# Kernel optimization log

Measured on AMD Instinct MI355X. Metric: run time of the kernel, lower is better.

Reference implementation:

```python
import jax, jax.numpy as jnp
import numpy as np

N_NODES = 64
KS = (52, 42, 34)  # ceil(0.8*64), ceil(0.8*52), ceil(0.8*42)


def _gcn(x, A, W, b):
    # GCNConv(improved=True): self-loop fill 2.0, symmetric normalization. A[tgt, src], weighted.
    n = A.shape[0]
    Ah = A + 2.0 * jnp.eye(n, dtype=A.dtype)
    d = Ah.sum(-1)
    dis = jnp.where(d > 0, jax.lax.rsqrt(d), 0.0)
    An = dis[:, None] * Ah * dis[None, :]
    return An @ (x @ W) + b


def _augment(A):
    # GraphUNet.augment_adj: add self loops (weight 1), A2 = A1 @ A1, remove self loops
    n = A.shape[0]
    eye = jnp.eye(n, dtype=A.dtype)
    A1 = A + eye
    return (A1 @ A1) * (1.0 - eye)


def _pool(x, A, w, k):
    # TopKPooling: score = tanh(x.w/||w||), keep top-k, scale kept features by score
    s = jnp.tanh((x @ w) / jnp.linalg.norm(w))
    sv, perm = jax.lax.top_k(s, k)
    return x[perm] * sv[:, None], A[perm][:, perm], perm


def _unet(x, A, dw0, db0, dws, dbs, pws, uws, ubs, uwl, ubl):
    # GraphUNet(depth=3, sum_res=True), single graph: x [n, F2], A [n, n]
    x = jax.nn.relu(_gcn(x, A, dw0, db0))
    xs, As, perms = [x], [A], []
    for i in range(3):
        A = _augment(A)
        x, A, perm = _pool(x, A, pws[i], KS[i])
        x = jax.nn.relu(_gcn(x, A, dws[i], dbs[i]))
        if i < 2:
            xs.append(x)
            As.append(A)
        perms.append(perm)
    for i in range(3):
        j = 2 - i
        res, Aj, perm = xs[j], As[j], perms[j]
        x = res + jnp.zeros_like(res).at[perm].set(x)
        if i < 2:
            x = jax.nn.relu(_gcn(x, Aj, uws[i], ubs[i]))
        else:
            x = _gcn(x, Aj, uwl, ubl)
    return x


def _nnconv(x, src, dst, ea, mw, mb, rw, bias):
    # NNConv(aggr='mean'): per-edge MLP weight, gather-matmul-scatter-mean + root + bias
    B, E = src.shape
    fin, fout = rw.shape
    We = jax.nn.relu(ea @ mw + mb).reshape(B, E, fin, fout)  # [B,E,fin,fout]
    xs = jnp.take_along_axis(x, src[..., None], axis=1)      # [B,E,fin]
    msg = jnp.einsum('bei,beio->beo', xs, We)                # [B,E,fout]
    seg = jax.vmap(lambda m, d: jax.ops.segment_sum(m, d, num_segments=N_NODES))
    sums = seg(msg, dst)
    cnt = seg(jnp.ones(msg.shape[:2] + (1,), msg.dtype), dst)
    agg = sums / jnp.maximum(cnt, 1.0)
    return agg + x @ rw + bias


def _adj(src, dst):
    A = jnp.zeros((N_NODES, N_NODES), jnp.float32).at[dst, src].set(1.0)
    return A * (1.0 - jnp.eye(N_NODES, dtype=jnp.float32))


def _branch(x, ei, ea, mlp1, mlp2, u1, u2):
    src, dst = ei[:, 0], ei[:, 1]
    A = jax.vmap(_adj)(src, dst)
    x = jax.nn.relu(_nnconv(x, src, dst, ea, *mlp1))
    x = jax.nn.relu(jax.vmap(lambda h, a: _unet(h, a, *u1))(x, A))
    x = jax.nn.relu(_nnconv(x, src, dst, ea, *mlp2))
    x = jax.nn.relu(jax.vmap(lambda h, a: _unet(h, a, *u2))(x, A))
    return x.mean(axis=1)  # global_mean_pool (equal-sized graphs)


def setup_inputs() -> dict:
    key = jax.random.key(0)
    keys = iter(jax.random.split(key, 64))
    def nrm(shape, s=1.0):
        return jax.random.normal(next(keys), shape, jnp.float32) * s
    B, n, E, F, F2, Q, H, C = 128, 64, 512, 64, 32, 16, 256, 50
    inp = {}
    inp['x1'] = nrm((B, n, F))
    inp['ei1'] = jax.random.randint(next(keys), (B, 2, E), 0, n, jnp.int32)
    inp['ea1'] = jax.random.uniform(next(keys), (B, E, 1), jnp.float32)
    inp['jw1'] = nrm((B, Q))
    inp['x2'] = nrm((B, n, F))
    inp['ei2'] = jax.random.randint(next(keys), (B, 2, E), 0, n, jnp.int32)
    inp['ea2'] = jax.random.uniform(next(keys), (B, E, 1), jnp.float32)
    inp['jw2'] = nrm((B, Q))
    inp['m1w'] = nrm((1, F * F2), 0.1)
    inp['m1b'] = nrm((F * F2,), 0.1)
    inp['r1w'] = nrm((F, F2), 0.1)
    inp['c1b'] = nrm((F2,), 0.1)
    inp['m2w'] = nrm((1, F2 * F2), 0.1)
    inp['m2b'] = nrm((F2 * F2,), 0.1)
    inp['r2w'] = nrm((F2, F2), 0.1)
    inp['c2b'] = nrm((F2,), 0.1)
    for p in ('u1', 'u2'):
        inp[p + '_dw0'] = nrm((F2, C), 0.1)
        inp[p + '_db0'] = nrm((C,), 0.1)
        inp[p + '_dws'] = nrm((3, C, C), 0.1)
        inp[p + '_dbs'] = nrm((3, C), 0.1)
        inp[p + '_pws'] = nrm((3, C), 0.1)
        inp[p + '_uws'] = nrm((2, C, C), 0.1)
        inp[p + '_ubs'] = nrm((2, C), 0.1)
        inp[p + '_uwl'] = nrm((C, F2), 0.1)
        inp[p + '_ubl'] = nrm((F2,), 0.1)
    inp['bb_w'] = nrm(((F2 + Q) * 2, H), 0.1)
    inp['bb_b'] = nrm((H,), 0.1)
    return inp


def reference(x1, ei1, ea1, jw1, x2, ei2, ea2, jw2,
              m1w, m1b, r1w, c1b, m2w, m2b, r2w, c2b,
              u1_dw0, u1_db0, u1_dws, u1_dbs, u1_pws, u1_uws, u1_ubs, u1_uwl, u1_ubl,
              u2_dw0, u2_db0, u2_dws, u2_dbs, u2_pws, u2_uws, u2_ubs, u2_uwl, u2_ubl,
              bb_w, bb_b):
    mlp1 = (m1w, m1b, r1w, c1b)
    mlp2 = (m2w, m2b, r2w, c2b)
    u1 = (u1_dw0, u1_db0, u1_dws, u1_dbs, u1_pws, u1_uws, u1_ubs, u1_uwl, u1_ubl)
    u2 = (u2_dw0, u2_db0, u2_dws, u2_dbs, u2_pws, u2_uws, u2_ubs, u2_uwl, u2_ubl)
    r1 = _branch(x1, ei1, ea1, mlp1, mlp2, u1, u2)
    r2 = _branch(x2, ei2, ea2, mlp1, mlp2, u1, u2)
    c = jnp.concatenate([r1, jw1, r2, jw2], axis=1)  # [(F2+Q)*2]
    return jax.nn.relu(c @ bb_w + bb_b)
```

## Files before the change

kernel.cpp:

```cpp
#include <hip/hip_runtime.h>
#include <math.h>

#define UT 1024
#define XS 52
#define ASTR 66

__device__ __forceinline__ float wred16(float v) {
    v += __shfl_xor(v, 8); v += __shfl_xor(v, 4);
    v += __shfl_xor(v, 2); v += __shfl_xor(v, 1);
    return v;
}

__device__ __forceinline__ void gcn_u(int n, int cin, int cout,
    float* __restrict__ x, float* __restrict__ tmp,
    const float* __restrict__ A, float* __restrict__ Wl,
    float* __restrict__ dis,
    const float* __restrict__ Wg, const float* __restrict__ bg, bool relu)
{
    const int tid = threadIdx.x;
    const int nso = (cout + 3) >> 2;
    for (int idx = tid; idx < 51 * 52; idx += UT) {
        int r = idx / 52, c = idx - r * 52;
        float v = 0.f;
        if (r < cin && c < cout) v = Wg[r * cout + c];
        else if (r == 50 && c < cout) v = bg[c];
        Wl[idx] = v;
    }
    {
        int r = tid >> 4, l = tid & 15;
        float s = 0.f;
        if (r < n) for (int j = l; j < n; j += 16) s += A[r * ASTR + j];
        s = wred16(s);
        if (l == 0 && r < n) dis[r] = 1.0f / sqrtf(2.0f + s);
    }
    __syncthreads();
    const int nr2 = n >> 1;
    const int items = nr2 * nso;
    for (int it = tid; it < items; it += UT) {
        int i0 = (it / nso) * 2, o0 = (it - (it / nso) * nso) * 4;
        float a0=0,a1=0,a2=0,a3=0, b0=0,b1=0,b2=0,b3=0;
        float c0=0,c1=0,c2=0,c3=0, d0=0,d1=0,d2=0,d3=0;
        for (int k = 0; k < cin; k += 2) {
            float4 w0 = *(const float4*)&Wl[k * 52 + o0];
            float4 w1 = *(const float4*)&Wl[(k + 1) * 52 + o0];
            float2 xa = *(const float2*)&x[i0 * XS + k];
            float2 xb = *(const float2*)&x[(i0 + 1) * XS + k];
            a0 = fmaf(xa.x, w0.x, a0); a1 = fmaf(xa.x, w0.y, a1);
            a2 = fmaf(xa.x, w0.z, a2); a3 = fmaf(xa.x, w0.w, a3);
            b0 = fmaf(xa.y, w1.x, b0); b1 = fmaf(xa.y, w1.y, b1);
            b2 = fmaf(xa.y, w1.z, b2); b3 = fmaf(xa.y, w1.w, b3);
            c0 = fmaf(xb.x, w0.x, c0); c1 = fmaf(xb.x, w0.y, c1);
            c2 = fmaf(xb.x, w0.z, c2); c3 = fmaf(xb.x, w0.w, c3);
            d0 = fmaf(xb.y, w1.x, d0); d1 = fmaf(xb.y, w1.y, d1);
            d2 = fmaf(xb.y, w1.z, d2); d3 = fmaf(xb.y, w1.w, d3);
        }
        float e0 = dis[i0], e1 = dis[i0 + 1];
        float4 t0, t1;
        t0.x = (a0 + b0) * e0; t0.y = (a1 + b1) * e0;
        t0.z = (a2 + b2) * e0; t0.w = (a3 + b3) * e0;
        t1.x = (c0 + d0) * e1; t1.y = (c1 + d1) * e1;
        t1.z = (c2 + d2) * e1; t1.w = (c3 + d3) * e1;
        *(float4*)&tmp[i0 * XS + o0] = t0;
        *(float4*)&tmp[(i0 + 1) * XS + o0] = t1;
    }
    __syncthreads();
    for (int it = tid; it < items; it += UT) {
        int i0 = (it / nso) * 2, o0 = (it - (it / nso) * nso) * 4;
        float a0=0,a1=0,a2=0,a3=0, b0=0,b1=0,b2=0,b3=0;
        float c0=0,c1=0,c2=0,c3=0, d0=0,d1=0,d2=0,d3=0;
        for (int j = 0; j < n; j += 2) {
            float4 t0 = *(const float4*)&tmp[j * XS + o0];
            float4 t1 = *(const float4*)&tmp[(j + 1) * XS + o0];
            float2 Aa2 = *(const float2*)&A[i0 * ASTR + j];
            float2 Ab2 = *(const float2*)&A[(i0 + 1) * ASTR + j];
            a0 = fmaf(Aa2.x, t0.x, a0); a1 = fmaf(Aa2.x, t0.y, a1);
            a2 = fmaf(Aa2.x, t0.z, a2); a3 = fmaf(Aa2.x, t0.w, a3);
            b0 = fmaf(Aa2.y, t1.x, b0); b1 = fmaf(Aa2.y, t1.y, b1);
            b2 = fmaf(Aa2.y, t1.z, b2); b3 = fmaf(Aa2.y, t1.w, b3);
            c0 = fmaf(Ab2.x, t0.x, c0); c1 = fmaf(Ab2.x, t0.y, c1);
            c2 = fmaf(Ab2.x, t0.z, c2); c3 = fmaf(Ab2.x, t0.w, c3);
            d0 = fmaf(Ab2.y, t1.x, d0); d1 = fmaf(Ab2.y, t1.y, d1);
            d2 = fmaf(Ab2.y, t1.z, d2); d3 = fmaf(Ab2.y, t1.w, d3);
        }
        float4 bias = *(const float4*)&Wl[50 * 52 + o0];
        float4 s0 = *(const float4*)&tmp[i0 * XS + o0];
        float4 s1 = *(const float4*)&tmp[(i0 + 1) * XS + o0];
        float e0 = dis[i0], e1 = dis[i0 + 1];
        float4 r0, r1;
        r0.x = fmaf(e0, (a0 + b0) + 2.f * s0.x, bias.x);
        r0.y = fmaf(e0, (a1 + b1) + 2.f * s0.y, bias.y);
        r0.z = fmaf(e0, (a2 + b2) + 2.f * s0.z, bias.z);
        r0.w = fmaf(e0, (a3 + b3) + 2.f * s0.w, bias.w);
        r1.x = fmaf(e1, (c0 + d0) + 2.f * s1.x, bias.x);
        r1.y = fmaf(e1, (c1 + d1) + 2.f * s1.y, bias.y);
        r1.z = fmaf(e1, (c2 + d2) + 2.f * s1.z, bias.z);
        r1.w = fmaf(e1, (c3 + d3) + 2.f * s1.w, bias.w);
        if (relu) {
            r0.x = fmaxf(r0.x, 0.f); r0.y = fmaxf(r0.y, 0.f);
            r0.z = fmaxf(r0.z, 0.f); r0.w = fmaxf(r0.w, 0.f);
            r1.x = fmaxf(r1.x, 0.f); r1.y = fmaxf(r1.y, 0.f);
            r1.z = fmaxf(r1.z, 0.f); r1.w = fmaxf(r1.w, 0.f);
        }
        *(float4*)&x[i0 * XS + o0] = r0;
        *(float4*)&x[(i0 + 1) * XS + o0] = r1;
    }
    __syncthreads();
}

__device__ __forceinline__ void gcn_sparse(int cin, int cout,
    float* __restrict__ x, float* __restrict__ tmp,
    const int* __restrict__ csrOff, const int* __restrict__ csrCol,
    float* __restrict__ dis0, float* __restrict__ Wl,
    const float* __restrict__ Wg, const float* __restrict__ bg, bool relu)
{
    const int tid = threadIdx.x;
    const int nso = (cout + 3) >> 2;
    for (int idx = tid; idx < 51 * 52; idx += UT) {
        int r = idx / 52, c = idx - r * 52;
        float v = 0.f;
        if (r < cin && c < cout) v = Wg[r * cout + c];
        else if (r == 50 && c < cout) v = bg[c];
        Wl[idx] = v;
    }
    if (tid < 64)
        dis0[tid] = 1.0f / sqrtf(2.0f + (float)(csrOff[tid + 1] - csrOff[tid]));
    __syncthreads();
    const int items1 = 32 * nso;
    if (tid < items1) {
        int i0 = (tid / nso) * 2, o0 = (tid - (tid / nso) * nso) * 4;
        float a0=0,a1=0,a2=0,a3=0, b0=0,b1=0,b2=0,b3=0;
        float c0=0,c1=0,c2=0,c3=0, d0=0,d1=0,d2=0,d3=0;
        for (int k = 0; k < cin; k += 2) {
            float4 w0 = *(const float4*)&Wl[k * 52 + o0];
            float4 w1 = *(const float4*)&Wl[(k + 1) * 52 + o0];
            float2 xa = *(const float2*)&x[i0 * XS + k];
            float2 xb = *(const float2*)&x[(i0 + 1) * XS + k];
            a0 = fmaf(xa.x, w0.x, a0); a1 = fmaf(xa.x, w0.y, a1);
            a2 = fmaf(xa.x, w0.z, a2); a3 = fmaf(xa.x, w0.w, a3);
            b0 = fmaf(xa.y, w1.x, b0); b1 = fmaf(xa.y, w1.y, b1);
            b2 = fmaf(xa.y, w1.z, b2); b3 = fmaf(xa.y, w1.w, b3);
            c0 = fmaf(xb.x, w0.x, c0); c1 = fmaf(xb.x, w0.y, c1);
            c2 = fmaf(xb.x, w0.z, c2); c3 = fmaf(xb.x, w0.w, c3);
            d0 = fmaf(xb.y, w1.x, d0); d1 = fmaf(xb.y, w1.y, d1);
            d2 = fmaf(xb.y, w1.z, d2); d3 = fmaf(xb.y, w1.w, d3);
        }
        float e0 = dis0[i0], e1 = dis0[i0 + 1];
        float4 t0, t1;
        t0.x = (a0 + b0) * e0; t0.y = (a1 + b1) * e0;
        t0.z = (a2 + b2) * e0; t0.w = (a3 + b3) * e0;
        t1.x = (c0 + d0) * e1; t1.y = (c1 + d1) * e1;
        t1.z = (c2 + d2) * e1; t1.w = (c3 + d3) * e1;
        *(float4*)&tmp[i0 * XS + o0] = t0;
        *(float4*)&tmp[(i0 + 1) * XS + o0] = t1;
    }
    __syncthreads();
    const int items = 64 * nso;
    if (tid < items) {
        int i = tid / nso, o0 = (tid - i * nso) * 4;
        int base = csrOff[i], end = csrOff[i + 1];
        float a0 = 0.f, a1 = 0.f, a2 = 0.f, a3 = 0.f;
        for (int p = base; p < end; p++) {
            int j = csrCol[p];
            float4 t = *(const float4*)&tmp[j * XS + o0];
            a0 += t.x; a1 += t.y; a2 += t.z; a3 += t.w;
        }
        float4 bias = *(const float4*)&Wl[50 * 52 + o0];
        float4 s0 = *(const float4*)&tmp[i * XS + o0];
        float d = dis0[i];
        float4 r;
        r.x = fmaf(d, a0 + 2.f * s0.x, bias.x);
        r.y = fmaf(d, a1 + 2.f * s0.y, bias.y);
        r.z = fmaf(d, a2 + 2.f * s0.z, bias.z);
        r.w = fmaf(d, a3 + 2.f * s0.w, bias.w);
        if (relu) {
            r.x = fmaxf(r.x, 0.f); r.y = fmaxf(r.y, 0.f);
            r.z = fmaxf(r.z, 0.f); r.w = fmaxf(r.w, 0.f);
        }
        *(float4*)&x[i * XS + o0] = r;
    }
    __syncthreads();
}

__device__ __forceinline__ void down_scores(int n, const float* __restrict__ wg,
                                            const float* __restrict__ px,
                                            float* __restrict__ scr)
{
    const int tid = threadIdx.x;
    int r = tid >> 4, l = tid & 15;
    float s = 0.f, wn = 0.f;
    for (int q = l; q < 50; q += 16) {
        float wv = wg[q];
        wn = fmaf(wv, wv, wn);
        s  = fmaf(px[r * XS + q], wv, s);
    }
    s = wred16(s); wn = wred16(wn);
    if (l == 0 && r < n) scr[r] = tanhf(s / sqrtf(wn));
}

__device__ __forceinline__ void down_rest(int n, int kk,
    float* __restrict__ px, float* __restrict__ pt_,
    float* __restrict__ pA, float* __restrict__ pF,
    float* __restrict__ scr, float* __restrict__ dis, float* __restrict__ svals,
    int* __restrict__ perm, const float* __restrict__ dw,
    const float* __restrict__ db)
{
    const int tid = threadIdx.x;
    __syncthreads();
    if (tid < 64) {
        float v = (tid < n) ? scr[tid] : -2.0f;
        int id = tid;
        for (int sz = 2; sz <= 64; sz <<= 1)
            for (int st = sz >> 1; st > 0; st >>= 1) {
                float ov = __shfl_xor(v, st);
                int oi = __shfl_xor(id, st);
                bool up = ((tid & sz) == 0);
                bool lower = ((tid & st) == 0);
                bool less = (v > ov) || (v == ov && id < oi);
                bool keep = (up == lower) ? less : !less;
                if (!keep) { v = ov; id = oi; }
            }
        if (tid < kk) { perm[tid] = id; svals[tid] = v; }
    }
    __syncthreads();
    for (int idx = tid; idx < n * 13; idx += UT) {
        int m = idx / 13, u0 = (idx - (idx / 13) * 13) * 4;
        float4 gv;
        gv.x = (u0 + 0 < kk) ? pA[m * ASTR + perm[u0 + 0]] : 0.f;
        gv.y = (u0 + 1 < kk) ? pA[m * ASTR + perm[u0 + 1]] : 0.f;
        gv.z = (u0 + 2 < kk) ? pA[m * ASTR + perm[u0 + 2]] : 0.f;
        gv.w = (u0 + 3 < kk) ? pA[m * ASTR + perm[u0 + 3]] : 0.f;
        *(float4*)&pt_[m * XS + u0] = gv;
    }
    float gx0=0, gx1=0, gx2=0, gx3=0; int gdst = -1;
    if (tid < kk * 13) {
        int t = tid / 13, q0 = (tid - t * 13) * 4;
        float sv = svals[t]; int p = perm[t];
        gx0 = px[p * XS + q0 + 0] * sv; gx1 = px[p * XS + q0 + 1] * sv;
        gx2 = px[p * XS + q0 + 2] * sv; gx3 = px[p * XS + q0 + 3] * sv;
        gdst = t * XS + q0;
    }
    __syncthreads();
    if (gdst >= 0) {
        px[gdst] = gx0; px[gdst + 1] = gx1; px[gdst + 2] = gx2; px[gdst + 3] = gx3;
    }
    int nst = (kk + 3) >> 2, kt2 = kk >> 1;
    for (int it = tid; it < kt2 * nst; it += UT) {
        int t0 = (it / nst) * 2, u0 = (it - (it / nst) * nst) * 4;
        int p0 = perm[t0], p1 = perm[t0 + 1];
        float a0=0,a1=0,a2=0,a3=0, b0=0,b1=0,b2=0,b3=0;
        float c0=0,c1=0,c2=0,c3=0, d0=0,d1=0,d2=0,d3=0;
        for (int m = 0; m < n; m += 2) {
            float4 g0 = *(const float4*)&pt_[m * XS + u0];
            float4 g1 = *(const float4*)&pt_[(m + 1) * XS + u0];
            float2 q0v = *(const float2*)&pA[p0 * ASTR + m];
            float2 q1v = *(const float2*)&pA[p1 * ASTR + m];
            a0 = fmaf(q0v.x, g0.x, a0); a1 = fmaf(q0v.x, g0.y, a1);
            a2 = fmaf(q0v.x, g0.z, a2); a3 = fmaf(q0v.x, g0.w, a3);
            b0 = fmaf(q0v.y, g1.x, b0); b1 = fmaf(q0v.y, g1.y, b1);
            b2 = fmaf(q0v.y, g1.z, b2); b3 = fmaf(q0v.y, g1.w, b3);
            c0 = fmaf(q1v.x, g0.x, c0); c1 = fmaf(q1v.x, g0.y, c1);
            c2 = fmaf(q1v.x, g0.z, c2); c3 = fmaf(q1v.x, g0.w, c3);
            d0 = fmaf(q1v.y, g1.x, d0); d1 = fmaf(q1v.y, g1.y, d1);
            d2 = fmaf(q1v.y, g1.z, d2); d3 = fmaf(q1v.y, g1.w, d3);
        }
        float4 gg0 = *(const float4*)&pt_[p0 * XS + u0];
        float4 gg1 = *(const float4*)&pt_[p1 * XS + u0];
        float v;
        v = (a0 + b0) + 2.f * gg0.x; pF[t0 * ASTR + u0 + 0] = (u0 + 0 == t0) ? 0.f : v;
        v = (a1 + b1) + 2.f * gg0.y; pF[t0 * ASTR + u0 + 1] = (u0 + 1 == t0) ? 0.f : v;
        v = (a2 + b2) + 2.f * gg0.z; pF[t0 * ASTR + u0 + 2] = (u0 + 2 == t0) ? 0.f : v;
        v = (a3 + b3) + 2.f * gg0.w; pF[t0 * ASTR + u0 + 3] = (u0 + 3 == t0) ? 0.f : v;
        v = (c0 + d0) + 2.f * gg1.x; pF[(t0+1) * ASTR + u0 + 0] = (u0 + 0 == t0+1) ? 0.f : v;
        v = (c1 + d1) + 2.f * gg1.y; pF[(t0+1) * ASTR + u0 + 1] = (u0 + 1 == t0+1) ? 0.f : v;
        v = (c2 + d2) + 2.f * gg1.z; pF[(t0+1) * ASTR + u0 + 2] = (u0 + 2 == t0+1) ? 0.f : v;
        v = (c3 + d3) + 2.f * gg1.w; pF[(t0+1) * ASTR + u0 + 3] = (u0 + 3 == t0+1) ? 0.f : v;
    }
    __syncthreads();
    gcn_u(kk, 50, 50, px, pt_, pF, pA, dis, dw, db, true);
}

__global__ __launch_bounds__(UT)
void unet_kernel(const float* __restrict__ xin, const float* __restrict__ wsA,
                 const int* __restrict__ wsCsrO, const int* __restrict__ wsCsrC,
                 const float* __restrict__ dw0, const float* __restrict__ db0,
                 const float* __restrict__ dws, const float* __restrict__ dbs,
                 const float* __restrict__ pws,
                 const float* __restrict__ uws, const float* __restrict__ ubs,
                 const float* __restrict__ uwl, const float* __restrict__ ubl,
                 float* __restrict__ ws_xs, float* __restrict__ ws_As,
                 float* __restrict__ outp, int mean_mode)
{
    const int g = blockIdx.x, tid = threadIdx.x;
    __shared__ __align__(16) float Aa[64 * ASTR];
    __shared__ __align__(16) float Ab[64 * ASTR];
    __shared__ __align__(16) float x0c[64 * XS];
    __shared__ __align__(16) float x1c[64 * XS];
    __shared__ float scr[64];
    __shared__ float dis[64];
    __shared__ float dis0[64];
    __shared__ float svals[64];
    __shared__ int   permL[192];
    __shared__ int   csrOffL[65];
    __shared__ int   csrColL[512];

    float *pA = Aa, *pF = Ab, *px = x0c, *pt_ = x1c;
    float* xs_g = ws_xs + (size_t)g * 9984;
    float* as_g = ws_As + (size_t)g * 6208;
    const float* wsAg = wsA + (size_t)g * 4224;
    const int nsz[4] = {64, 52, 42, 34};

    {
        const float* xg = xin + (size_t)g * 2048;
        for (int idx = tid; idx < 512; idx += UT) {
            int i = idx >> 3, o0 = (idx & 7) * 4;
            *(float4*)&px[i * XS + o0] = *(const float4*)&xg[i * 32 + o0];
        }
        for (int idx = tid; idx < 4224; idx += UT) pA[idx] = wsAg[idx];
        if (tid < 65) csrOffL[tid] = wsCsrO[(size_t)g * 66 + tid];
        if (tid >= 128 && tid < 640) csrColL[tid - 128] = wsCsrC[(size_t)g * 512 + tid - 128];
    }
    __syncthreads();

    gcn_sparse(32, 50, px, pt_, csrOffL, csrColL, dis0, pF, dw0, db0, true);

    for (int lvl = 0; lvl < 3; lvl++) {
        int n = nsz[lvl], kk = nsz[lvl + 1];
        down_scores(n, pws + lvl * 50, px, scr);
        {
            float* xd = xs_g + lvl * 3328;
            for (int idx = tid; idx < 3328; idx += UT) xd[idx] = px[idx];
            if (lvl == 1) for (int idx = tid; idx < 3432; idx += UT) as_g[idx] = pA[idx];
            if (lvl == 2) for (int idx = tid; idx < 2772; idx += UT) as_g[3432 + idx] = pA[idx];
        }
        down_rest(n, kk, px, pt_, pA, pF, scr, dis, svals, permL + lvl * 64,
                  dws + lvl * 2500, dbs + lvl * 50);
        { float* t = pA; pA = pF; pF = t; }
    }

    for (int i2 = 0; i2 < 3; i2++) {
        int j = 2 - i2;
        int kc = nsz[j + 1];
        {
            const float* resg = xs_g + j * 3328;
            for (int idx = tid; idx < 3328; idx += UT) pt_[idx] = resg[idx];
            if (j == 1) {
                for (int idx = tid; idx < 3432; idx += UT) pF[idx] = as_g[idx];
            } else if (j == 2) {
                for (int idx = tid; idx < 2772; idx += UT) pF[idx] = as_g[3432 + idx];
            }
        }
        __syncthreads();
        const int* perm = permL + j * 64;
        for (int it = tid; it < kc * 13; it += UT) {
            int t = it / 13, q0 = (it - t * 13) * 4;
            int p = perm[t];
            pt_[p*XS+q0+0] += px[t*XS+q0+0]; pt_[p*XS+q0+1] += px[t*XS+q0+1];
            pt_[p*XS+q0+2] += px[t*XS+q0+2]; pt_[p*XS+q0+3] += px[t*XS+q0+3];
        }
        __syncthreads();
        if (i2 < 2)
            gcn_u(nsz[j], 50, 50, pt_, px, pF, pA, dis, uws + i2 * 2500, ubs + i2 * 50, true);
        else
            gcn_sparse(50, 32, pt_, px, csrOffL, csrColL, dis0, pF, uwl, ubl, false);
        { float* t2 = px; px = pt_; pt_ = t2; }
        { float* t2 = pA; pA = pF; pF = t2; }
    }

    if (mean_mode) {
        int r = tid >> 4, l = tid & 15;
        if (r < 32) {
            float s = 0.f;
            for (int i = l; i < 64; i += 16) s += fmaxf(px[i * XS + r], 0.f);
            s = wred16(s);
            if (l == 0) outp[(size_t)g * 32 + r] = s * (1.0f / 64.0f);
        }
    } else {
        float* og = outp + (size_t)g * 2048;
        for (int idx = tid; idx < 512; idx += UT) {
            int i = idx >> 3, o0 = (idx & 7) * 4;
            float4 vv = *(const float4*)&px[i * XS + o0];
            vv.x = fmaxf(vv.x, 0.f); vv.y = fmaxf(vv.y, 0.f);
            vv.z = fmaxf(vv.z, 0.f); vv.w = fmaxf(vv.w, 0.f);
            *(float4*)&og[i * 32 + o0] = vv;
        }
    }
}

template<int FIN>
__device__ __forceinline__ void nnconv_core(
    const float* __restrict__ xl, const float* __restrict__ rwl,
    float* __restrict__ agg,
    const int* __restrict__ dOff, const int* __restrict__ sSrc,
    const float* __restrict__ sEa,
    const float* __restrict__ mw, const float* __restrict__ mb,
    const float* __restrict__ bias, float* __restrict__ xout_g)
{
    constexpr int CH = FIN / 2;
    const int tid = threadIdx.x;
    const int o = tid & 31, ic = (tid >> 5) & 1, wv = tid >> 6;
    float mwr[CH], mbr[CH];
    #pragma unroll
    for (int z = 0; z < CH; z++) {
        mwr[z] = mw[(ic * CH + z) * 32 + o];
        mbr[z] = mb[(ic * CH + z) * 32 + o];
    }
    for (int dd = 0; dd < 4; dd++) {
        int d = wv * 4 + dd;
        int b = dOff[d], e = dOff[d + 1];
        float ac0 = 0.f, ac1 = 0.f, ac2 = 0.f, ac3 = 0.f;
        for (int p = b; p < e; p++) {
            int s = sSrc[p];
            float av = sEa[p];
            #pragma unroll
            for (int z = 0; z < CH; z += 4) {
                float4 xv = *(const float4*)&xl[s * FIN + ic * CH + z];
                ac0 = fmaf(xv.x, fmaxf(fmaf(av, mwr[z + 0], mbr[z + 0]), 0.f), ac0);
                ac1 = fmaf(xv.y, fmaxf(fmaf(av, mwr[z + 1], mbr[z + 1]), 0.f), ac1);
                ac2 = fmaf(xv.z, fmaxf(fmaf(av, mwr[z + 2], mbr[z + 2]), 0.f), ac2);
                ac3 = fmaf(xv.w, fmaxf(fmaf(av, mwr[z + 3], mbr[z + 3]), 0.f), ac3);
            }
        }
        float acc = (ac0 + ac1) + (ac2 + ac3);
        acc += __shfl_down(acc, 32);
        if (ic == 0) agg[d * 32 + o] = acc;
    }
    __syncthreads();
    {
        int nn = tid >> 4, o0 = (tid & 15) * 2;
        float a0 = 0.f, a1 = 0.f, b0 = 0.f, b1 = 0.f;
        for (int i = 0; i < FIN; i += 2) {
            float xv0 = xl[nn * FIN + i], xv1 = xl[nn * FIN + i + 1];
            float2 w0 = *(const float2*)&rwl[i * 32 + o0];
            float2 w1 = *(const float2*)&rwl[(i + 1) * 32 + o0];
            a0 = fmaf(xv0, w0.x, a0); a1 = fmaf(xv0, w0.y, a1);
            b0 = fmaf(xv1, w1.x, b0); b1 = fmaf(xv1, w1.y, b1);
        }
        float cn  = (float)(dOff[nn + 1] - dOff[nn]);
        float inv = 1.0f / fmaxf(cn, 1.f);
        float2 sv = *(const float2*)&agg[nn * 32 + o0];
        xout_g[nn * 32 + o0]     = fmaxf(fmaf(sv.x, inv, (a0 + b0) + bias[o0]),     0.f);
        xout_g[nn * 32 + o0 + 1] = fmaxf(fmaf(sv.y, inv, (a1 + b1) + bias[o0 + 1]), 0.f);
    }
}

__global__ __launch_bounds__(UT)
void nnconv1_kernel(const float* __restrict__ x1, const float* __restrict__ x2,
                    const int* __restrict__ ei1, const int* __restrict__ ei2,
                    const float* __restrict__ ea1, const float* __restrict__ ea2,
                    const float* __restrict__ mw, const float* __restrict__ mb,
                    const float* __restrict__ rw, const float* __restrict__ bias,
                    float* __restrict__ wsA, int* __restrict__ wsEdg,
                    int* __restrict__ wsCsrO, int* __restrict__ wsCsrC,
                    float* __restrict__ xout)
{
    const int g = blockIdx.x, tid = threadIdx.x;
    __shared__ __align__(16) float xl[4096];
    __shared__ __align__(16) float rwl[2048];
    __shared__ __align__(16) float agg[2048];
    __shared__ __align__(16) float Al[64 * ASTR];
    __shared__ int   srcl[512];
    __shared__ int   dstl[512];
    __shared__ float eal[512];
    __shared__ int   sSrc[512];
    __shared__ float sEaL[512];
    __shared__ int   sTot[64];
    __shared__ int   dOff[65];
    __shared__ int   rowc[64];
    __shared__ int   csrOffL[65];

    const float* xg; const int* eig; const float* eag;
    if (g < 128) {
        xg = x1 + (size_t)g * 4096; eig = ei1 + (size_t)g * 1024; eag = ea1 + (size_t)g * 512;
    } else {
        int h = g - 128;
        xg = x2 + (size_t)h * 4096; eig = ei2 + (size_t)h * 1024; eag = ea2 + (size_t)h * 512;
    }
    int* chunkCnt = (int*)agg;

    *(float4*)&xl[tid * 4] = *(const float4*)&xg[tid * 4];
    if (tid < 512) { srcl[tid] = eig[tid]; dstl[tid] = eig[512 + tid]; eal[tid] = eag[tid]; }
    for (int i = tid; i < 64 * ASTR; i += UT) Al[i] = 0.f;
    chunkCnt[tid] = 0;
    __syncthreads();
    if (tid < 512) {
        Al[dstl[tid] * ASTR + srcl[tid]] = 1.f;
        atomicAdd(&chunkCnt[(tid >> 5) * 64 + dstl[tid]], 1);
    }
    __syncthreads();
    if (tid < 64) {
        Al[tid * ASTR + tid] = 0.f;
        int run = 0;
        for (int c = 0; c < 16; c++) {
            int t = chunkCnt[c * 64 + tid];
            chunkCnt[c * 64 + tid] = run; run += t;
        }
        sTot[tid] = run;
    }
    __syncthreads();
    if (tid < 64) {
        int v = sTot[tid]; int x = v;
        #pragma unroll
        for (int dl = 1; dl < 64; dl <<= 1) {
            int y = __shfl_up(x, dl);
            if (tid >= dl) x += y;
        }
        dOff[tid] = x - v;
        if (tid == 63) dOff[64] = x;
    }
    if (tid >= 64 && tid < 128) {
        int i = tid - 64; int c = 0;
        for (int j = 0; j < 64; j++) c += (Al[i * ASTR + j] != 0.f) ? 1 : 0;
        rowc[i] = c;
    }
    for (int i = tid; i < 2048; i += UT) rwl[i] = rw[i];
    for (int i = tid; i < 64 * ASTR; i += UT) wsA[(size_t)g * 4224 + i] = Al[i];
    __syncthreads();
    if (tid < 64) {
        int v = rowc[tid]; int x = v;
        #pragma unroll
        for (int dl = 1; dl < 64; dl <<= 1) {
            int y = __shfl_up(x, dl);
            if (tid >= dl) x += y;
        }
        csrOffL[tid] = x - v;
        if (tid == 63) csrOffL[64] = x;
    }
    if (tid < 512) {
        int dk = dstl[tid]; int c = tid >> 5; int lr = 0;
        for (int e2 = (c << 5); e2 < tid; e2++) lr += (dstl[e2] == dk) ? 1 : 0;
        int pos = dOff[dk] + chunkCnt[c * 64 + dk] + lr;
        sSrc[pos] = srcl[tid]; sEaL[pos] = eal[tid];
    }
    __syncthreads();
    if (tid < 64) {
        int p = csrOffL[tid];
        for (int j = 0; j < 64; j++)
            if (Al[tid * ASTR + j] != 0.f) wsCsrC[(size_t)g * 512 + (p++)] = j;
    }
    if (tid >= 64 && tid < 129) wsCsrO[(size_t)g * 66 + (tid - 64)] = csrOffL[tid - 64];
    if (tid >= 192 && tid < 257) wsEdg[(size_t)g * 1152 + (tid - 192)] = dOff[tid - 192];
    if (tid < 512) {
        wsEdg[(size_t)g * 1152 + 66 + tid] = sSrc[tid];
        ((float*)wsEdg)[(size_t)g * 1152 + 578 + tid] = sEaL[tid];
    }
    __syncthreads();

    nnconv_core<64>(xl, rwl, agg, dOff, sSrc, sEaL, mw, mb, bias,
                    xout + (size_t)g * 2048);
}

__global__ __launch_bounds__(UT)
void nnconv2_kernel(const float* __restrict__ xin,
                    const int* __restrict__ wsEdg,
                    const float* __restrict__ mw, const float* __restrict__ mb,
                    const float* __restrict__ rw, const float* __restrict__ bias,
                    float* __restrict__ xout)
{
    const int g = blockIdx.x, tid = threadIdx.x;
    __shared__ __align__(16) float xl[2048];
    __shared__ __align__(16) float rwl[1024];
    __shared__ __align__(16) float agg[2048];
    __shared__ int   dOff[65];
    __shared__ int   sSrc[512];
    __shared__ float sEaL[512];

    const float* xg = xin + (size_t)g * 2048;
    if (tid < 512) *(float4*)&xl[tid * 4] = *(const float4*)&xg[tid * 4];
    if (tid < 1024) rwl[tid] = rw[tid];
    if (tid < 65) dOff[tid] = wsEdg[(size_t)g * 1152 + tid];
    if (tid >= 128 && tid < 640) {
        sSrc[tid - 128] = wsEdg[(size_t)g * 1152 + 66 + (tid - 128)];
        sEaL[tid - 128] = ((const float*)wsEdg)[(size_t)g * 1152 + 578 + (tid - 128)];
    }
    __syncthreads();

    nnconv_core<32>(xl, rwl, agg, dOff, sSrc, sEaL, mw, mb, bias,
                    xout + (size_t)g * 2048);
}

__global__ __launch_bounds__(256)
void head_kernel(const float* __restrict__ r,
                 const float* __restrict__ jw1, const float* __restrict__ jw2,
                 const float* __restrict__ bw, const float* __restrict__ bb,
                 float* __restrict__ out)
{
    const int b = blockIdx.x, h = threadIdx.x;
    float acc = bb[h];
    const float* r1 = r + (size_t)b * 32;
    const float* r2 = r + (size_t)(128 + b) * 32;
    #pragma unroll
    for (int q = 0; q < 32; q++) acc += r1[q] * bw[q * 256 + h];
    #pragma unroll
    for (int q = 0; q < 16; q++) acc += jw1[b * 16 + q] * bw[(32 + q) * 256 + h];
    #pragma unroll
    for (int q = 0; q < 32; q++) acc += r2[q] * bw[(48 + q) * 256 + h];
    #pragma unroll
    for (int q = 0; q < 16; q++) acc += jw2[b * 16 + q] * bw[(80 + q) * 256 + h];
    out[(size_t)b * 256 + h] = fmaxf(acc, 0.f);
}

extern "C" void kernel_launch(void* const* d_in, const int* in_sizes, int n_in,
                              void* d_out, int out_size, void* d_ws, size_t ws_size,
                              hipStream_t stream)
{
    const float* x1  = (const float*)d_in[0];
    const int*   ei1 = (const int*)  d_in[1];
    const float* ea1 = (const float*)d_in[2];
    const float* jw1 = (const float*)d_in[3];
    const float* x2  = (const float*)d_in[4];
    const int*   ei2 = (const int*)  d_in[5];
    const float* ea2 = (const float*)d_in[6];
    const float* jw2 = (const float*)d_in[7];
    const float* m1w = (const float*)d_in[8];
    const float* m1b = (const float*)d_in[9];
    const float* r1w = (const float*)d_in[10];
    const float* c1b = (const float*)d_in[11];
    const float* m2w = (const float*)d_in[12];
    const float* m2b = (const float*)d_in[13];
    const float* r2w = (const float*)d_in[14];
    const float* c2b = (const float*)d_in[15];
    const float* u1p[9]; for (int i = 0; i < 9; i++) u1p[i] = (const float*)d_in[16 + i];
    const float* u2p[9]; for (int i = 0; i < 9; i++) u2p[i] = (const float*)d_in[25 + i];
    const float* bbw = (const float*)d_in[34];
    const float* bbb = (const float*)d_in[35];

    char* ws = (char*)d_ws;
    size_t off = 0;
    float* wsA  = (float*)(ws + off); off += 256ull * 4224 * 4;
    float* xc1  = (float*)(ws + off); off += 256ull * 2048 * 4;
    float* xu1  = (float*)(ws + off); off += 256ull * 2048 * 4;
    float* xc2  = (float*)(ws + off); off += 256ull * 2048 * 4;
    float* rr   = (float*)(ws + off); off += 256ull * 32 * 4;
    float* wxs  = (float*)(ws + off); off += 256ull * 9984 * 4;
    float* wAs  = (float*)(ws + off); off += 256ull * 6208 * 4;
    int*   wEdg = (int*)  (ws + off); off += 256ull * 1152 * 4;
    int*   wCsO = (int*)  (ws + off); off += 256ull * 66 * 4;
    int*   wCsC = (int*)  (ws + off); off += 256ull * 512 * 4;
    (void)ws_size; (void)in_sizes; (void)n_in; (void)out_size;

    nnconv1_kernel<<<256, UT, 0, stream>>>(x1, x2, ei1, ei2, ea1, ea2,
                                           m1w, m1b, r1w, c1b,
                                           wsA, wEdg, wCsO, wCsC, xc1);
    unet_kernel<<<256, UT, 0, stream>>>(xc1, wsA, wCsO, wCsC,
        u1p[0], u1p[1], u1p[2], u1p[3], u1p[4], u1p[5], u1p[6], u1p[7], u1p[8],
        wxs, wAs, xu1, 0);
    nnconv2_kernel<<<256, UT, 0, stream>>>(xu1, wEdg, m2w, m2b, r2w, c2b, xc2);
    unet_kernel<<<256, UT, 0, stream>>>(xc2, wsA, wCsO, wCsC,
        u2p[0], u2p[1], u2p[2], u2p[3], u2p[4], u2p[5], u2p[6], u2p[7], u2p[8],
        wxs, wAs, rr, 1);
    head_kernel<<<128, 256, 0, stream>>>(rr, jw1, jw2, bbw, bbb, (float*)d_out);
}
```

Measured before the change: 311.1 us.

## Fuse nnconv1, first UNet and nnconv2 into one kernel via shared smem

```diff
diff --git a/kernel.cpp b/kernel.cpp
--- a/kernel.cpp
+++ b/kernel.cpp
@@ -4,6 +4,19 @@
 #define UT 1024
 #define XS 52
 #define ASTR 66
+
+#define SA    0
+#define SB    4224
+#define SX0   8448
+#define SX1   11776
+#define SSCR  15104
+#define SDIS  15168
+#define SDIS0 15232
+#define SSVL  15296
+#define SPERM 15360
+#define SCSRO 15552
+#define SCSRC 15617
+#define SMSZ  16160
 
 __device__ __forceinline__ float wred16(float v) {
     v += __shfl_xor(v, 8); v += __shfl_xor(v, 4);
@@ -279,47 +292,39 @@
     gcn_u(kk, 50, 50, px, pt_, pF, pA, dis, dw, db, true);
 }
 
-__global__ __launch_bounds__(UT)
-void unet_kernel(const float* __restrict__ xin, const float* __restrict__ wsA,
-                 const int* __restrict__ wsCsrO, const int* __restrict__ wsCsrC,
-                 const float* __restrict__ dw0, const float* __restrict__ db0,
-                 const float* __restrict__ dws, const float* __restrict__ dbs,
-                 const float* __restrict__ pws,
-                 const float* __restrict__ uws, const float* __restrict__ ubs,
-                 const float* __restrict__ uwl, const float* __restrict__ ubl,
-                 float* __restrict__ ws_xs, float* __restrict__ ws_As,
-                 float* __restrict__ outp, int mean_mode)
-{
-    const int g = blockIdx.x, tid = threadIdx.x;
-    __shared__ __align__(16) float Aa[64 * ASTR];
-    __shared__ __align__(16) float Ab[64 * ASTR];
-    __shared__ __align__(16) float x0c[64 * XS];
-    __shared__ __align__(16) float x1c[64 * XS];
-    __shared__ float scr[64];
-    __shared__ float dis[64];
-    __shared__ float dis0[64];
-    __shared__ float svals[64];
-    __shared__ int   permL[192];
-    __shared__ int   csrOffL[65];
-    __shared__ int   csrColL[512];
+__device__ void unet_body(float* __restrict__ smem,
+    const float* __restrict__ xin, const float* __restrict__ wsAg,
+    const int* __restrict__ wsCsrO, const int* __restrict__ wsCsrC,
+    const float* __restrict__ dw0, const float* __restrict__ db0,
+    const float* __restrict__ dws, const float* __restrict__ dbs,
+    const float* __restrict__ pws,
+    const float* __restrict__ uws, const float* __restrict__ ubs,
+    const float* __restrict__ uwl, const float* __restrict__ ubl,
+    float* __restrict__ xs_g, float* __restrict__ as_g,
+    float* __restrict__ outp, int g, int mean_mode)
+{
+    const int tid = threadIdx.x;
+    float* Aa  = smem + SA;  float* Ab  = smem + SB;
+    float* x0c = smem + SX0; float* x1c = smem + SX1;
+    float* scr = smem + SSCR; float* dis = smem + SDIS;
+    float* dis0 = smem + SDIS0; float* svals = smem + SSVL;
+    int* permL = (int*)(smem + SPERM);
+    int* csrOffL = (int*)(smem + SCSRO);
+    int* csrColL = (int*)(smem + SCSRC);
 
     float *pA = Aa, *pF = Ab, *px = x0c, *pt_ = x1c;
-    float* xs_g = ws_xs + (size_t)g * 9984;
-    float* as_g = ws_As + (size_t)g * 6208;
-    const float* wsAg = wsA + (size_t)g * 4224;
     const int nsz[4] = {64, 52, 42, 34};
 
-    {
-        const float* xg = xin + (size_t)g * 2048;
+    if (xin) {
         for (int idx = tid; idx < 512; idx += UT) {
             int i = idx >> 3, o0 = (idx & 7) * 4;
-            *(float4*)&px[i * XS + o0] = *(const float4*)&xg[i * 32 + o0];
+            *(float4*)&px[i * XS + o0] = *(const float4*)&xin[i * 32 + o0];
         }
         for (int idx = tid; idx < 4224; idx += UT) pA[idx] = wsAg[idx];
-        if (tid < 65) csrOffL[tid] = wsCsrO[(size_t)g * 66 + tid];
-        if (tid >= 128 && tid < 640) csrColL[tid - 128] = wsCsrC[(size_t)g * 512 + tid - 128];
-    }
-    __syncthreads();
+        if (tid < 65) csrOffL[tid] = wsCsrO[tid];
+        if (tid >= 128 && tid < 640) csrColL[tid - 128] = wsCsrC[tid - 128];
+        __syncthreads();
+    }
 
     gcn_sparse(32, 50, px, pt_, csrOffL, csrColL, dis0, pF, dw0, db0, true);
 
@@ -366,7 +371,7 @@
         { float* t2 = pA; pA = pF; pF = t2; }
     }
 
-    if (mean_mode) {
+    if (mean_mode == 1) {
         int r = tid >> 4, l = tid & 15;
         if (r < 32) {
             float s = 0.f;
@@ -374,15 +379,7 @@
             s = wred16(s);
             if (l == 0) outp[(size_t)g * 32 + r] = s * (1.0f / 64.0f);
         }
-    } else {
-        float* og = outp + (size_t)g * 2048;
-        for (int idx = tid; idx < 512; idx += UT) {
-            int i = idx >> 3, o0 = (idx & 7) * 4;
-            float4 vv = *(const float4*)&px[i * XS + o0];
-            vv.x = fmaxf(vv.x, 0.f); vv.y = fmaxf(vv.y, 0.f);
-            vv.z = fmaxf(vv.z, 0.f); vv.w = fmaxf(vv.w, 0.f);
-            *(float4*)&og[i * 32 + o0] = vv;
-        }
+        __syncthreads();
     }
 }
 
@@ -393,7 +390,7 @@
     const int* __restrict__ dOff, const int* __restrict__ sSrc,
     const float* __restrict__ sEa,
     const float* __restrict__ mw, const float* __restrict__ mb,
-    const float* __restrict__ bias, float* __restrict__ xout_g)
+    const float* __restrict__ bias, float* __restrict__ out, int ostride)
 {
     constexpr int CH = FIN / 2;
     const int tid = threadIdx.x;
@@ -438,35 +435,51 @@
         float cn  = (float)(dOff[nn + 1] - dOff[nn]);
         float inv = 1.0f / fmaxf(cn, 1.f);
         float2 sv = *(const float2*)&agg[nn * 32 + o0];
-        xout_g[nn * 32 + o0]     = fmaxf(fmaf(sv.x, inv, (a0 + b0) + bias[o0]),     0.f);
-        xout_g[nn * 32 + o0 + 1] = fmaxf(fmaf(sv.y, inv, (a1 + b1) + bias[o0 + 1]), 0.f);
-    }
+        float r0 = fmaxf(fmaf(sv.x, inv, (a0 + b0) + bias[o0]),     0.f);
+        float r1 = fmaxf(fmaf(sv.y, inv, (a1 + b1) + bias[o0 + 1]), 0.f);
+        __syncthreads();
+        out[nn * ostride + o0]     = r0;
+        out[nn * ostride + o0 + 1] = r1;
+    }
+    __syncthreads();
 }
 
 __global__ __launch_bounds__(UT)
-void nnconv1_kernel(const float* __restrict__ x1, const float* __restrict__ x2,
-                    const int* __restrict__ ei1, const int* __restrict__ ei2,
-                    const float* __restrict__ ea1, const float* __restrict__ ea2,
-                    const float* __restrict__ mw, const float* __restrict__ mb,
-                    const float* __restrict__ rw, const float* __restrict__ bias,
-                    float* __restrict__ wsA, int* __restrict__ wsEdg,
-                    int* __restrict__ wsCsrO, int* __restrict__ wsCsrC,
-                    float* __restrict__ xout)
+void fused1_kernel(const float* __restrict__ x1, const float* __restrict__ x2,
+                   const int* __restrict__ ei1, const int* __restrict__ ei2,
+                   const float* __restrict__ ea1, const float* __restrict__ ea2,
+                   const float* __restrict__ m1w, const float* __restrict__ m1b,
+                   const float* __restrict__ r1w, const float* __restrict__ c1b,
+                   const float* __restrict__ m2w, const float* __restrict__ m2b,
+                   const float* __restrict__ r2w, const float* __restrict__ c2b,
+                   const float* __restrict__ u0, const float* __restrict__ u1,
+                   const float* __restrict__ u2, const float* __restrict__ u3,
+                   const float* __restrict__ u4, const float* __restrict__ u5,
+                   const float* __restrict__ u6, const float* __restrict__ u7,
+                   const float* __restrict__ u8,
+                   float* __restrict__ wsA, int* __restrict__ wsEdg,
+                   int* __restrict__ wsCsrO, int* __restrict__ wsCsrC,
+                   float* __restrict__ ws_xs, float* __restrict__ ws_As,
+                   float* __restrict__ xc2)
 {
     const int g = blockIdx.x, tid = threadIdx.x;
-    __shared__ __align__(16) float xl[4096];
-    __shared__ __align__(16) float rwl[2048];
-    __shared__ __align__(16) float agg[2048];
-    __shared__ __align__(16) float Al[64 * ASTR];
-    __shared__ int   srcl[512];
-    __shared__ int   dstl[512];
-    __shared__ float eal[512];
-    __shared__ int   sSrc[512];
-    __shared__ float sEaL[512];
-    __shared__ int   sTot[64];
-    __shared__ int   dOff[65];
-    __shared__ int   rowc[64];
-    __shared__ int   csrOffL[65];
+    __shared__ __align__(16) float smem[SMSZ];
+
+    float* Al   = smem + SA;
+    float* xl   = smem + SB;
+    int*   srcl = (int*)(smem + SX0);
+    int*   dstl = (int*)(smem + SX0 + 512);
+    float* eal  = smem + SX0 + 1024;
+    int*   chunkCnt = (int*)(smem + SX0 + 1536);
+    int*   sTot = (int*)(smem + SX0 + 2560);
+    int*   rowc = (int*)(smem + SX0 + 2624);
+    float* rwl  = smem + SX1;
+    int*   dOff = (int*)(smem + SX1 + 2048);
+    int*   sSrc = (int*)(smem + SX1 + 2113);
+    float* sEa  = smem + SX1 + 2625;
+    float* agg  = smem + SX0;
+    int*   csrOffL = (int*)(smem + SCSRO);
+    int*   csrColL = (int*)(smem + SCSRC);
 
     const float* xg; const int* eig; const float* eag;
     if (g < 128) {
@@ -475,11 +488,10 @@
         int h = g - 128;
         xg = x2 + (size_t)h * 4096; eig = ei2 + (size_t)h * 1024; eag = ea2 + (size_t)h * 512;
     }
-    int* chunkCnt = (int*)agg;
 
     *(float4*)&xl[tid * 4] = *(const float4*)&xg[tid * 4];
     if (tid < 512) { srcl[tid] = eig[tid]; dstl[tid] = eig[512 + tid]; eal[tid] = eag[tid]; }
-    for (int i = tid; i < 64 * ASTR; i += UT) Al[i] = 0.f;
+    for (int i = tid; i < 4224; i += UT) Al[i] = 0.f;
     chunkCnt[tid] = 0;
     __syncthreads();
     if (tid < 512) {
@@ -512,8 +524,8 @@
         for (int j = 0; j < 64; j++) c += (Al[i * ASTR + j] != 0.f) ? 1 : 0;
         rowc[i] = c;
     }
-    for (int i = tid; i < 2048; i += UT) rwl[i] = rw[i];
-    for (int i = tid; i < 64 * ASTR; i += UT) wsA[(size_t)g * 4224 + i] = Al[i];
+    for (int i = tid; i < 2048; i += UT) rwl[i] = r1w[i];
+    for (int i = tid; i < 4224; i += UT) wsA[(size_t)g * 4224 + i] = Al[i];
     __syncthreads();
     if (tid < 64) {
         int v = rowc[tid]; int x = v;
@@ -525,57 +537,79 @@
         csrOffL[tid] = x - v;
         if (tid == 63) csrOffL[64] = x;
     }
+    __syncthreads();
     if (tid < 512) {
         int dk = dstl[tid]; int c = tid >> 5; int lr = 0;
         for (int e2 = (c << 5); e2 < tid; e2++) lr += (dstl[e2] == dk) ? 1 : 0;
         int pos = dOff[dk] + chunkCnt[c * 64 + dk] + lr;
-        sSrc[pos] = srcl[tid]; sEaL[pos] = eal[tid];
+        sSrc[pos] = srcl[tid]; sEa[pos] = eal[tid];
     }
     __syncthreads();
     if (tid < 64) {
         int p = csrOffL[tid];
         for (int j = 0; j < 64; j++)
-            if (Al[tid * ASTR + j] != 0.f) wsCsrC[(size_t)g * 512 + (p++)] = j;
+            if (Al[tid * ASTR + j] != 0.f) {
+                csrColL[p] = j;
+                wsCsrC[(size_t)g * 512 + p] = j;
+                p++;
+            }
     }
     if (tid >= 64 && tid < 129) wsCsrO[(size_t)g * 66 + (tid - 64)] = csrOffL[tid - 64];
     if (tid >= 192 && tid < 257) wsEdg[(size_t)g * 1152 + (tid - 192)] = dOff[tid - 192];
     if (tid < 512) {
         wsEdg[(size_t)g * 1152 + 66 + tid] = sSrc[tid];
-        ((float*)wsEdg)[(size_t)g * 1152 + 578 + tid] = sEaL[tid];
-    }
-    __syncthreads();
-
-    nnconv_core<64>(xl, rwl, agg, dOff, sSrc, sEaL, mw, mb, bias,
-                    xout + (size_t)g * 2048);
+        ((float*)wsEdg)[(size_t)g * 1152 + 578 + tid] = sEa[tid];
+    }
+    __syncthreads();
+
+    nnconv_core<64>(xl, rwl, agg, dOff, sSrc, sEa, m1w, m1b, c1b,
+                    smem + SX0, XS);
+
+    unet_body(smem, nullptr, nullptr, nullptr, nullptr,
+              u0, u1, u2, u3, u4, u5, u6, u7, u8,
+              ws_xs + (size_t)g * 9984, ws_As + (size_t)g * 6208,
+              nullptr, g, -1);
+
+    float* xl2  = smem + SA;
+    int*   dOff2 = (int*)(smem + SA + 2048);
+    int*   sSrc2 = (int*)(smem + SA + 2113);
+    float* sEa2  = smem + SA + 2625;
+    float* rwl2  = smem + SB;
+    float* agg2  = smem + SB + 1024;
+    {
+        const float* xf = smem + SX1;
+        for (int idx = tid; idx < 2048; idx += UT)
+            xl2[idx] = fmaxf(xf[(idx >> 5) * XS + (idx & 31)], 0.f);
+        if (tid < 1024) rwl2[tid] = r2w[tid];
+        if (tid < 65) dOff2[tid] = wsEdg[(size_t)g * 1152 + tid];
+        if (tid >= 128 && tid < 640) {
+            sSrc2[tid - 128] = wsEdg[(size_t)g * 1152 + 66 + (tid - 128)];
+            sEa2[tid - 128]  = ((const float*)wsEdg)[(size_t)g * 1152 + 578 + (tid - 128)];
+        }
+    }
+    __syncthreads();
+    nnconv_core<32>(xl2, rwl2, agg2, dOff2, sSrc2, sEa2, m2w, m2b, c2b,
+                    xc2 + (size_t)g * 2048, 32);
 }
 
 __global__ __launch_bounds__(UT)
-void nnconv2_kernel(const float* __restrict__ xin,
-                    const int* __restrict__ wsEdg,
-                    const float* __restrict__ mw, const float* __restrict__ mb,
-                    const float* __restrict__ rw, const float* __restrict__ bias,
-                    float* __restrict__ xout)
-{
-    const int g = blockIdx.x, tid = threadIdx.x;
-    __shared__ __align__(16) float xl[2048];
-    __shared__ __align__(16) float rwl[1024];
-    __shared__ __align__(16) float agg[2048];
-    __shared__ int   dOff[65];
-    __shared__ int   sSrc[512];
-    __shared__ float sEaL[512];
-
-    const float* xg = xin + (size_t)g * 2048;
-    if (tid < 512) *(float4*)&xl[tid * 4] = *(const float4*)&xg[tid * 4];
-    if (tid < 1024) rwl[tid] = rw[tid];
-    if (tid < 65) dOff[tid] = wsEdg[(size_t)g * 1152 + tid];
-    if (tid >= 128 && tid < 640) {
-        sSrc[tid - 128] = wsEdg[(size_t)g * 1152 + 66 + (tid - 128)];
-        sEaL[tid - 128] = ((const float*)wsEdg)[(size_t)g * 1152 + 578 + (tid - 128)];
-    }
-    __syncthreads();
-
-    nnconv_core<32>(xl, rwl, agg, dOff, sSrc, sEaL, mw, mb, bias,
-                    xout + (size_t)g * 2048);
+void unet2_kernel(const float* __restrict__ xc2, const float* __restrict__ wsA,
+                  const int* __restrict__ wsCsrO, const int* __restrict__ wsCsrC,
+                  const float* __restrict__ u0, const float* __restrict__ u1,
+                  const float* __restrict__ u2, const float* __restrict__ u3,
+                  const float* __restrict__ u4, const float* __restrict__ u5,
+                  const float* __restrict__ u6, const float* __restrict__ u7,
+                  const float* __restrict__ u8,
+                  float* __restrict__ ws_xs, float* __restrict__ ws_As,
+                  float* __restrict__ rr)
+{
+    const int g = blockIdx.x;
+    __shared__ __align__(16) float smem[SMSZ];
+    unet_body(smem, xc2 + (size_t)g * 2048, wsA + (size_t)g * 4224,
+              wsCsrO + (size_t)g * 66, wsCsrC + (size_t)g * 512,
+              u0, u1, u2, u3, u4, u5, u6, u7, u8,
+              ws_xs + (size_t)g * 9984, ws_As + (size_t)g * 6208,
+              rr, g, 1);
 }
 
 __global__ __launch_bounds__(256)
@@ -627,26 +661,22 @@
     char* ws = (char*)d_ws;
     size_t off = 0;
     float* wsA  = (float*)(ws + off); off += 256ull * 4224 * 4;
-    float* xc1  = (float*)(ws + off); off += 256ull * 2048 * 4;
-    float* xu1  = (float*)(ws + off); off += 256ull * 2048 * 4;
-    float* xc2  = (float*)(ws + off); off += 256ull * 2048 * 4;
-    float* rr   = (float*)(ws + off); off += 256ull * 32 * 4;
     float* wxs  = (float*)(ws + off); off += 256ull * 9984 * 4;
     float* wAs  = (float*)(ws + off); off += 256ull * 6208 * 4;
     int*   wEdg = (int*)  (ws + off); off += 256ull * 1152 * 4;
     int*   wCsO = (int*)  (ws + off); off += 256ull * 66 * 4;
     int*   wCsC = (int*)  (ws + off); off += 256ull * 512 * 4;
+    float* xc2  = (float*)(ws + off); off += 256ull * 2048 * 4;
+    float* rr   = (float*)(ws + off); off += 256ull * 32 * 4;
     (void)ws_size; (void)in_sizes; (void)n_in; (void)out_size;
 
-    nnconv1_kernel<<<256, UT, 0, stream>>>(x1, x2, ei1, ei2, ea1, ea2,
-                                           m1w, m1b, r1w, c1b,
-                                           wsA, wEdg, wCsO, wCsC, xc1);
-    unet_kernel<<<256, UT, 0, stream>>>(xc1, wsA, wCsO, wCsC,
+    fused1_kernel<<<256, UT, 0, stream>>>(
+        x1, x2, ei1, ei2, ea1, ea2,
+        m1w, m1b, r1w, c1b, m2w, m2b, r2w, c2b,
         u1p[0], u1p[1], u1p[2], u1p[3], u1p[4], u1p[5], u1p[6], u1p[7], u1p[8],
-        wxs, wAs, xu1, 0);
-    nnconv2_kernel<<<256, UT, 0, stream>>>(xu1, wEdg, m2w, m2b, r2w, c2b, xc2);
-    unet_kernel<<<256, UT, 0, stream>>>(xc2, wsA, wCsO, wCsC,
+        wsA, wEdg, wCsO, wCsC, wxs, wAs, xc2);
+    unet2_kernel<<<256, UT, 0, stream>>>(xc2, wsA, wCsO, wCsC,
         u2p[0], u2p[1], u2p[2], u2p[3], u2p[4], u2p[5], u2p[6], u2p[7], u2p[8],
-        wxs, wAs, rr, 1);
+        wxs, wAs, rr);
     head_kernel<<<128, 256, 0, stream>>>(rr, jw1, jw2, bbw, bbb, (float*)d_out);
 }
```

Result: slower. 376.9 us (+21.2%).
